# Kernel tuning notes

Measured on AMD Instinct MI355X. Metric: run time of the kernel, lower is better.

The kernel has to match this reference:

```python
import jax, jax.numpy as jnp
import numpy as np

N_SRC, N_DST, E = 10000, 40000, 1_280_000
IN_DIM, OUT_DIM, FEAT, O_DIM = 128, 64, 64, 300


def setup_inputs() -> dict:
    key = jax.random.key(0)
    ks = jax.random.split(key, 10)
    s = 0.05
    return {
        "h": jax.random.normal(ks[0], (N_SRC, IN_DIM), jnp.float32),
        "o": jax.random.normal(ks[1], (N_DST, O_DIM), jnp.float32),
        "tfidf": jax.random.normal(ks[2], (E, FEAT), jnp.float32),
        "W_fc": jax.random.normal(ks[3], (IN_DIM, OUT_DIM), jnp.float32) * s,
        "W_fc1": jax.random.normal(ks[4], (O_DIM, OUT_DIM), jnp.float32) * s,
        "W_feat": jax.random.normal(ks[5], (FEAT, OUT_DIM), jnp.float32) * s,
        "b_feat": jax.random.normal(ks[6], (OUT_DIM,), jnp.float32) * s,
        "W_attn": jax.random.normal(ks[7], (OUT_DIM, 1), jnp.float32) * s,
        "edge_src": jax.random.randint(ks[8], (E,), 0, N_SRC, jnp.int32),
        "edge_dst": jax.random.randint(ks[9], (E,), 0, N_DST, jnp.int32),
    }


def reference(h, o, tfidf, W_fc, W_fc1, W_feat, b_feat, W_attn, edge_src, edge_dst):
    n_dst = o.shape[0]
    # node projections: z on sentence (src) nodes via fc, on word (dst) nodes via fc1
    z_src = h @ W_fc                      # [N_SRC, D]
    z_dst = o @ W_fc1                     # [N_DST, D]
    # edge attention: z2 = src.z + dst.z + feat_fc(tfidfembed)
    dfeat = tfidf @ W_feat + b_feat       # [E, D]
    z2 = z_src[edge_src] + z_dst[edge_dst] + dfeat
    z3 = jnp.where(z2 > 0, z2, 0.01 * z2)  # leaky_relu, torch default slope
    e = (z3 @ W_attn)[:, 0]               # [E]
    # segment softmax over incoming edges of each dst (word) node
    m = jax.ops.segment_max(e, edge_dst, num_segments=n_dst)   # [N_DST]
    e_exp = jnp.exp(e - m[edge_dst])                           # [E]
    denom = jax.ops.segment_sum(e_exp, edge_dst, num_segments=n_dst)
    alpha = e_exp / jnp.maximum(denom, 1e-9)[edge_dst]         # [E]
    # weighted sum of src z into dst mailbox
    out = jax.ops.segment_sum(alpha[:, None] * z_src[edge_src], edge_dst,
                              num_segments=n_dst)              # [N_DST, D]
    return out
```

## Files before the change

### kernel.cpp

```cpp
#include <hip/hip_runtime.h>
#include <hip/hip_bf16.h>

#define N_SRC 10000
#define N_DST 40000
#define NE    1280000
#define IN_DIM 128
#define O_DIM  300
#define D      64
#define FEAT   64
#define NB     157

typedef __bf16 bf16x8 __attribute__((ext_vector_type(8)));
typedef __bf16 bf16x4 __attribute__((ext_vector_type(4)));
typedef float  f32x4  __attribute__((ext_vector_type(4)));

__global__ __launch_bounds__(256) void k_zsrc(const float* __restrict__ h,
                                              const float* __restrict__ Wfc,
                                              float* __restrict__ z,
                                              __bf16* __restrict__ zh){
    __shared__ float w[IN_DIM * D];
    for (int i = threadIdx.x; i < IN_DIM * D; i += blockDim.x) w[i] = Wfc[i];
    __syncthreads();
    int lane = threadIdx.x & 63;
    int wid  = blockIdx.x * 4 + (threadIdx.x >> 6);
    int nw   = gridDim.x * 4;
    for (int r0 = wid * 4; r0 < N_SRC; r0 += nw * 4){
        const f32x4* p0 = (const f32x4*)(h + (size_t)(r0 + 0) * IN_DIM);
        const f32x4* p1 = (const f32x4*)(h + (size_t)(r0 + 1) * IN_DIM);
        const f32x4* p2 = (const f32x4*)(h + (size_t)(r0 + 2) * IN_DIM);
        const f32x4* p3 = (const f32x4*)(h + (size_t)(r0 + 3) * IN_DIM);
        float a0 = 0.f, a1 = 0.f, a2 = 0.f, a3 = 0.f;
        #pragma unroll 4
        for (int k4 = 0; k4 < IN_DIM / 4; ++k4){
            f32x4 v0 = p0[k4], v1 = p1[k4], v2 = p2[k4], v3 = p3[k4];
            #pragma unroll
            for (int i = 0; i < 4; ++i){
                float wv = w[(k4 * 4 + i) * D + lane];
                a0 += v0[i] * wv; a1 += v1[i] * wv;
                a2 += v2[i] * wv; a3 += v3[i] * wv;
            }
        }
        z[(size_t)(r0 + 0) * D + lane] = a0; zh[(size_t)(r0 + 0) * D + lane] = (__bf16)a0;
        z[(size_t)(r0 + 1) * D + lane] = a1; zh[(size_t)(r0 + 1) * D + lane] = (__bf16)a1;
        z[(size_t)(r0 + 2) * D + lane] = a2; zh[(size_t)(r0 + 2) * D + lane] = (__bf16)a2;
        z[(size_t)(r0 + 3) * D + lane] = a3; zh[(size_t)(r0 + 3) * D + lane] = (__bf16)a3;
    }
}

__global__ __launch_bounds__(256) void k_zdst(const float* __restrict__ o,
                                              const float* __restrict__ Wfc1,
                                              float* __restrict__ z){
    extern __shared__ float w[];
    for (int i = threadIdx.x; i < O_DIM * D; i += blockDim.x) w[i] = Wfc1[i];
    __syncthreads();
    int lane = threadIdx.x & 63;
    int wid  = blockIdx.x * 4 + (threadIdx.x >> 6);
    int nw   = gridDim.x * 4;
    for (int r0 = wid * 4; r0 < N_DST; r0 += nw * 4){
        const f32x4* p0 = (const f32x4*)(o + (size_t)(r0 + 0) * O_DIM);
        const f32x4* p1 = (const f32x4*)(o + (size_t)(r0 + 1) * O_DIM);
        const f32x4* p2 = (const f32x4*)(o + (size_t)(r0 + 2) * O_DIM);
        const f32x4* p3 = (const f32x4*)(o + (size_t)(r0 + 3) * O_DIM);
        float a0 = 0.f, a1 = 0.f, a2 = 0.f, a3 = 0.f;
        #pragma unroll 5
        for (int k4 = 0; k4 < O_DIM / 4; ++k4){
            f32x4 v0 = p0[k4], v1 = p1[k4], v2 = p2[k4], v3 = p3[k4];
            #pragma unroll
            for (int i = 0; i < 4; ++i){
                float wv = w[(k4 * 4 + i) * D + lane];
                a0 += v0[i] * wv; a1 += v1[i] * wv;
                a2 += v2[i] * wv; a3 += v3[i] * wv;
            }
        }
        z[(size_t)(r0 + 0) * D + lane] = a0;
        z[(size_t)(r0 + 1) * D + lane] = a1;
        z[(size_t)(r0 + 2) * D + lane] = a2;
        z[(size_t)(r0 + 3) * D + lane] = a3;
    }
}

__global__ __launch_bounds__(256) void k_rank(const int* __restrict__ edst,
                                              int* __restrict__ cnt,
                                              int* __restrict__ rank){
    int i = blockIdx.x * blockDim.x + threadIdx.x;
    if (i < NE) rank[i] = atomicAdd(&cnt[edst[i]], 1);
}

__device__ __forceinline__ int block_incl_scan(int c, int* wsum){
    int lane = threadIdx.x & 63, w = threadIdx.x >> 6;
    int v = c;
    #pragma unroll
    for (int off = 1; off < 64; off <<= 1){
        int u = __shfl_up(v, off);
        if (lane >= off) v += u;
    }
    if (lane == 63) wsum[w] = v;
    __syncthreads();
    int add = 0;
    for (int ww = 0; ww < w; ++ww) add += wsum[ww];
    return v + add;
}

__global__ __launch_bounds__(256) void k_scan1(const int* __restrict__ cnt,
                                               int* __restrict__ bsum){
    __shared__ int wsum[4];
    int i = blockIdx.x * 256 + threadIdx.x;
    int c = (i < N_DST) ? cnt[i] : 0;
    int lane = threadIdx.x & 63, w = threadIdx.x >> 6;
    int v = c;
    #pragma unroll
    for (int off = 1; off < 64; off <<= 1) v += __shfl_xor(v, off);
    if (lane == 0) wsum[w] = v;
    __syncthreads();
    if (threadIdx.x == 0)
        bsum[blockIdx.x] = wsum[0] + wsum[1] + wsum[2] + wsum[3];
}

__global__ __launch_bounds__(256) void k_scan2(int* __restrict__ bsum){
    __shared__ int wsum[4];
    int i = threadIdx.x;
    int c = (i < NB) ? bsum[i] : 0;
    int v = block_incl_scan(c, wsum);
    if (i < NB) bsum[i] = v - c;
}

__global__ __launch_bounds__(256) void k_scan3(const int* __restrict__ cnt,
                                               const int* __restrict__ bsum,
                                               int* __restrict__ csr){
    __shared__ int wsum[4];
    int i = blockIdx.x * 256 + threadIdx.x;
    int c = (i < N_DST) ? cnt[i] : 0;
    int v = block_incl_scan(c, wsum);
    int val = bsum[blockIdx.x] + v - c;
    if (i < N_DST) csr[i] = val;
    if (blockIdx.x == 0 && threadIdx.x == 0) csr[N_DST] = NE;
}

__global__ __launch_bounds__(256) void k_edge(
        const float* __restrict__ tfidf,
        const int*   __restrict__ esrc, const int* __restrict__ edst,
        const int*   __restrict__ rank, const int* __restrict__ csr,
        const __bf16* __restrict__ zsrch, const float* __restrict__ zdst,
        const float* __restrict__ Wfeat, const float* __restrict__ bfeat,
        const float* __restrict__ Wattn,
        float* __restrict__ escore_p, int* __restrict__ ssrc_s){
    __shared__ __bf16 aw[8 * 64 * 8];
    for (int idx = threadIdx.x; idx < 64 * 64; idx += 256){
        int k = idx >> 6, m = idx & 63;
        int kh = k >> 5, r = k & 31, g2 = r >> 3, j = r & 7;
        int mt = m >> 4, lo2 = m & 15;
        aw[((((mt << 1) | kh) * 64) + ((g2 << 4) | lo2)) * 8 + j] = (__bf16)Wfeat[idx];
    }
    __syncthreads();

    int lane = threadIdx.x & 63;
    int lo = lane & 15, g = lane >> 4;

    f32x4 bf4[4], wa4[4];
    #pragma unroll
    for (int mt = 0; mt < 4; ++mt){
        int db = mt * 16 + g * 4;
        bf4[mt] = *(const f32x4*)(bfeat + db);
        wa4[mt] = *(const f32x4*)(Wattn + db);
    }

    const int NT = NE / 16;
    int wid = blockIdx.x * 4 + (threadIdx.x >> 6);
    int nw  = gridDim.x * 4;

    int tile = wid;
    if (tile >= NT) return;

    int e0 = tile * 16 + lo;
    int nss = __builtin_nontemporal_load(esrc + e0);
    int nsd = __builtin_nontemporal_load(edst + e0);
    int nrk = __builtin_nontemporal_load(rank + e0);
    int npos = csr[nsd] + nrk;
    {
        const float* tr = tfidf + (size_t)e0 * FEAT + g * 8;
    }
    const float* tr0 = tfidf + (size_t)e0 * FEAT + g * 8;
    f32x4 nfa0 = __builtin_nontemporal_load((const f32x4*)(tr0));
    f32x4 nfb0 = __builtin_nontemporal_load((const f32x4*)(tr0 + 4));
    f32x4 nfa1 = __builtin_nontemporal_load((const f32x4*)(tr0 + 32));
    f32x4 nfb1 = __builtin_nontemporal_load((const f32x4*)(tr0 + 36));

    for (; tile < NT; tile += nw){
        int css = nss, csd = nsd, cpos = npos;
        f32x4 fa0 = nfa0, fb0 = nfb0, fa1 = nfa1, fb1 = nfb1;

        bf16x4 zs[4]; f32x4 zd[4];
        #pragma unroll
        for (int mt = 0; mt < 4; ++mt){
            int db = mt * 16 + g * 4;
            zs[mt] = *(const bf16x4*)(zsrch + (size_t)css * D + db);
            zd[mt] = *(const f32x4*)(zdst  + (size_t)csd * D + db);
        }

        int tn = tile + nw;
        if (tn < NT){
            int en = tn * 16 + lo;
            nss = __builtin_nontemporal_load(esrc + en);
            nsd = __builtin_nontemporal_load(edst + en);
            nrk = __builtin_nontemporal_load(rank + en);
            npos = csr[nsd] + nrk;
            const float* trn = tfidf + (size_t)en * FEAT + g * 8;
            nfa0 = __builtin_nontemporal_load((const f32x4*)(trn));
            nfb0 = __builtin_nontemporal_load((const f32x4*)(trn + 4));
            nfa1 = __builtin_nontemporal_load((const f32x4*)(trn + 32));
            nfb1 = __builtin_nontemporal_load((const f32x4*)(trn + 36));
        }

        bf16x8 bfr[2];
        #pragma unroll
        for (int j = 0; j < 4; ++j){
            bfr[0][j]     = (__bf16)fa0[j];
            bfr[0][4 + j] = (__bf16)fb0[j];
            bfr[1][j]     = (__bf16)fa1[j];
            bfr[1][4 + j] = (__bf16)fb1[j];
        }

        float pacc = 0.f;
        #pragma unroll
        for (int mt = 0; mt < 4; ++mt){
            bf16x8 a0 = *(const bf16x8*)(aw + (((mt << 1) | 0) * 64 + lane) * 8);
            bf16x8 a1 = *(const bf16x8*)(aw + (((mt << 1) | 1) * 64 + lane) * 8);
            f32x4 acc = {0.f, 0.f, 0.f, 0.f};
            acc = __builtin_amdgcn_mfma_f32_16x16x32_bf16(a0, bfr[0], acc, 0, 0, 0);
            acc = __builtin_amdgcn_mfma_f32_16x16x32_bf16(a1, bfr[1], acc, 0, 0, 0);
            #pragma unroll
            for (int r = 0; r < 4; ++r){
                float z2 = acc[r] + (float)zs[mt][r] + zd[mt][r] + bf4[mt][r];
                float z3 = z2 > 0.f ? z2 : 0.01f * z2;
                pacc += z3 * wa4[mt][r];
            }
        }
        pacc += __shfl_xor(pacc, 16);
        pacc += __shfl_xor(pacc, 32);
        if (lane < 16){
            escore_p[cpos] = pacc;
            ssrc_s[cpos]   = css;
        }
    }
}

__global__ __launch_bounds__(256) void k_post(const int* __restrict__ csr,
                                              const int* __restrict__ ssrc,
                                              const float* __restrict__ escore_p,
                                              const float* __restrict__ zsrc,
                                              float* __restrict__ out){
    int lane = threadIdx.x & 63;
    int d    = blockIdx.x * 4 + (threadIdx.x >> 6);
    if (d >= N_DST) return;
    int beg = csr[d], end = csr[d + 1];

    float m = -3.4e38f;
    for (int j = beg + lane; j < end; j += 64)
        m = fmaxf(m, escore_p[j]);
    #pragma unroll
    for (int off = 1; off < 64; off <<= 1)
        m = fmaxf(m, __shfl_xor(m, off));

    float ssum = 0.f, acc = 0.f;
    for (int base = beg; base < end; base += 64){
        int n = end - base; if (n > 64) n = 64;
        int   sj = 0;
        float ej = 0.f;
        if (base + lane < end){
            sj = ssrc[base + lane];
            ej = __expf(escore_p[base + lane] - m);
        }
        ssum += ej;
        int t = 0;
        for (; t + 4 <= n; t += 4){
            int   s0 = __shfl(sj, t + 0), s1 = __shfl(sj, t + 1);
            int   s2 = __shfl(sj, t + 2), s3 = __shfl(sj, t + 3);
            float a0 = __shfl(ej, t + 0), a1 = __shfl(ej, t + 1);
            float a2 = __shfl(ej, t + 2), a3 = __shfl(ej, t + 3);
            float v0 = zsrc[(size_t)s0 * D + lane];
            float v1 = zsrc[(size_t)s1 * D + lane];
            float v2 = zsrc[(size_t)s2 * D + lane];
            float v3 = zsrc[(size_t)s3 * D + lane];
            acc += a0 * v0; acc += a1 * v1; acc += a2 * v2; acc += a3 * v3;
        }
        for (; t < n; ++t){
            int   s = __shfl(sj, t);
            float a = __shfl(ej, t);
            acc += a * zsrc[(size_t)s * D + lane];
        }
    }
    #pragma unroll
    for (int off = 1; off < 64; off <<= 1)
        ssum += __shfl_xor(ssum, off);
    float inv = 1.f / fmaxf(ssum, 1e-9f);
    out[(size_t)d * D + lane] = acc * inv;
}

extern "C" void kernel_launch(void* const* d_in, const int* in_sizes, int n_in,
                              void* d_out, int out_size, void* d_ws, size_t ws_size,
                              hipStream_t stream) {
    const float* h     = (const float*)d_in[0];
    const float* o     = (const float*)d_in[1];
    const float* tfidf = (const float*)d_in[2];
    const float* Wfc   = (const float*)d_in[3];
    const float* Wfc1  = (const float*)d_in[4];
    const float* Wfeat = (const float*)d_in[5];
    const float* bfeat = (const float*)d_in[6];
    const float* Wattn = (const float*)d_in[7];
    const int*   esrc  = (const int*)d_in[8];
    const int*   edst  = (const int*)d_in[9];
    float* out = (float*)d_out;

    float*  ws      = (float*)d_ws;
    float*  zsrc    = ws;
    float*  zdst    = ws + 640000;
    __bf16* zsrch   = (__bf16*)(ws + 3200000);
    float*  escorep = ws + 3520000;
    int*    ssrc    = (int*)(ws + 4800000);
    int*    rank    = (int*)(ws + 6080000);
    int*    cnt     = (int*)(ws + 7360000);
    int*    csr     = (int*)(ws + 7400000);
    int*    bsum    = (int*)(ws + 7440002);

    hipMemsetAsync(cnt, 0, N_DST * sizeof(int), stream);

    k_zsrc<<<256, 256, 0, stream>>>(h, Wfc, zsrc, zsrch);
    k_zdst<<<512, 256, O_DIM * D * sizeof(float), stream>>>(o, Wfc1, zdst);
    k_rank<<<NE / 256, 256, 0, stream>>>(edst, cnt, rank);
    k_scan1<<<NB, 256, 0, stream>>>(cnt, bsum);
    k_scan2<<<1, 256, 0, stream>>>(bsum);
    k_scan3<<<NB, 256, 0, stream>>>(cnt, bsum, csr);
    k_edge<<<2048, 256, 0, stream>>>(tfidf, esrc, edst, rank, csr, zsrch, zdst,
                                     Wfeat, bfeat, Wattn, escorep, ssrc);
    k_post<<<N_DST / 4, 256, 0, stream>>>(csr, ssrc, escorep, zsrc, out);
}
```

Measured before the change: 807.0 us.

## Drop softmax max pass, store edge-order scores with permutation, keep Wfeat in registers

The edge kernel now builds the Wfeat MFMA A-fragments directly in registers, which removes the LDS staging and the block barrier. It writes attention scores in original edge order, plus a CSR-ordered permutation of edge ids instead of the sorted source ids. The post kernel drops the segment-max pass and exponentiates the raw scores. It gathers the source id and score through the permutation, trading a sequential read pass for indirect, scattered loads. Removing the max subtraction relies on scores staying small enough that exp does not overflow.

```diff
diff --git a/kernel.cpp b/kernel.cpp
--- a/kernel.cpp
+++ b/kernel.cpp
@@ -143,19 +143,23 @@
         const __bf16* __restrict__ zsrch, const float* __restrict__ zdst,
         const float* __restrict__ Wfeat, const float* __restrict__ bfeat,
         const float* __restrict__ Wattn,
-        float* __restrict__ escore_p, int* __restrict__ ssrc_s){
-    __shared__ __bf16 aw[8 * 64 * 8];
-    for (int idx = threadIdx.x; idx < 64 * 64; idx += 256){
-        int k = idx >> 6, m = idx & 63;
-        int kh = k >> 5, r = k & 31, g2 = r >> 3, j = r & 7;
-        int mt = m >> 4, lo2 = m & 15;
-        aw[((((mt << 1) | kh) * 64) + ((g2 << 4) | lo2)) * 8 + j] = (__bf16)Wfeat[idx];
-    }
-    __syncthreads();
-
+        float* __restrict__ escore_e, int* __restrict__ sedge){
     int lane = threadIdx.x & 63;
     int lo = lane & 15, g = lane >> 4;
 
+    bf16x8 afr[4][2];
+    #pragma unroll
+    for (int mt = 0; mt < 4; ++mt){
+        int m = mt * 16 + lo;
+        #pragma unroll
+        for (int kh = 0; kh < 2; ++kh){
+            #pragma unroll
+            for (int j = 0; j < 8; ++j){
+                int k = kh * 32 + g * 8 + j;
+                afr[mt][kh][j] = (__bf16)Wfeat[k * D + m];
+            }
+        }
+    }
     f32x4 bf4[4], wa4[4];
     #pragma unroll
     for (int mt = 0; mt < 4; ++mt){
@@ -176,9 +180,6 @@
     int nsd = __builtin_nontemporal_load(edst + e0);
     int nrk = __builtin_nontemporal_load(rank + e0);
     int npos = csr[nsd] + nrk;
-    {
-        const float* tr = tfidf + (size_t)e0 * FEAT + g * 8;
-    }
     const float* tr0 = tfidf + (size_t)e0 * FEAT + g * 8;
     f32x4 nfa0 = __builtin_nontemporal_load((const f32x4*)(tr0));
     f32x4 nfb0 = __builtin_nontemporal_load((const f32x4*)(tr0 + 4));
@@ -223,11 +224,9 @@
         float pacc = 0.f;
         #pragma unroll
         for (int mt = 0; mt < 4; ++mt){
-            bf16x8 a0 = *(const bf16x8*)(aw + (((mt << 1) | 0) * 64 + lane) * 8);
-            bf16x8 a1 = *(const bf16x8*)(aw + (((mt << 1) | 1) * 64 + lane) * 8);
             f32x4 acc = {0.f, 0.f, 0.f, 0.f};
-            acc = __builtin_amdgcn_mfma_f32_16x16x32_bf16(a0, bfr[0], acc, 0, 0, 0);
-            acc = __builtin_amdgcn_mfma_f32_16x16x32_bf16(a1, bfr[1], acc, 0, 0, 0);
+            acc = __builtin_amdgcn_mfma_f32_16x16x32_bf16(afr[mt][0], bfr[0], acc, 0, 0, 0);
+            acc = __builtin_amdgcn_mfma_f32_16x16x32_bf16(afr[mt][1], bfr[1], acc, 0, 0, 0);
             #pragma unroll
             for (int r = 0; r < 4; ++r){
                 float z2 = acc[r] + (float)zs[mt][r] + zd[mt][r] + bf4[mt][r];
@@ -238,15 +237,16 @@
         pacc += __shfl_xor(pacc, 16);
         pacc += __shfl_xor(pacc, 32);
         if (lane < 16){
-            escore_p[cpos] = pacc;
-            ssrc_s[cpos]   = css;
+            escore_e[tile * 16 + lane] = pacc;
+            sedge[cpos] = tile * 16 + lane;
         }
     }
 }
 
 __global__ __launch_bounds__(256) void k_post(const int* __restrict__ csr,
-                                              const int* __restrict__ ssrc,
-                                              const float* __restrict__ escore_p,
+                                              const int* __restrict__ sedge,
+                                              const float* __restrict__ escore_e,
+                                              const int* __restrict__ esrc,
                                               const float* __restrict__ zsrc,
                                               float* __restrict__ out){
     int lane = threadIdx.x & 63;
@@ -254,21 +254,15 @@
     if (d >= N_DST) return;
     int beg = csr[d], end = csr[d + 1];
 
-    float m = -3.4e38f;
-    for (int j = beg + lane; j < end; j += 64)
-        m = fmaxf(m, escore_p[j]);
-    #pragma unroll
-    for (int off = 1; off < 64; off <<= 1)
-        m = fmaxf(m, __shfl_xor(m, off));
-
     float ssum = 0.f, acc = 0.f;
     for (int base = beg; base < end; base += 64){
         int n = end - base; if (n > 64) n = 64;
         int   sj = 0;
         float ej = 0.f;
         if (base + lane < end){
-            sj = ssrc[base + lane];
-            ej = __expf(escore_p[base + lane] - m);
+            int se = sedge[base + lane];
+            sj = esrc[se];
+            ej = __expf(escore_e[se]);
         }
         ssum += ej;
         int t = 0;
@@ -315,8 +309,8 @@
     float*  zsrc    = ws;
     float*  zdst    = ws + 640000;
     __bf16* zsrch   = (__bf16*)(ws + 3200000);
-    float*  escorep = ws + 3520000;
-    int*    ssrc    = (int*)(ws + 4800000);
+    float*  escoree = ws + 3520000;
+    int*    sedge   = (int*)(ws + 4800000);
     int*    rank    = (int*)(ws + 6080000);
     int*    cnt     = (int*)(ws + 7360000);
     int*    csr     = (int*)(ws + 7400000);
@@ -331,6 +325,6 @@
     k_scan2<<<1, 256, 0, stream>>>(bsum);
     k_scan3<<<NB, 256, 0, stream>>>(cnt, bsum, csr);
     k_edge<<<2048, 256, 0, stream>>>(tfidf, esrc, edst, rank, csr, zsrch, zdst,
-                                     Wfeat, bfeat, Wattn, escorep, ssrc);
-    k_post<<<N_DST / 4, 256, 0, stream>>>(csr, ssrc, escorep, zsrc, out);
-}
+                                     Wfeat, bfeat, Wattn, escoree, sedge);
+    k_post<<<N_DST / 4, 256, 0, stream>>>(csr, sedge, escoree, esrc, zsrc, out);
+}
```

After: 815.5 us. Within noise of the previous version (+1.1%).
